# Kernel optimization log

Measured on AMD Instinct MI355X. Metric: run time of the kernel, lower is better.

## Reference

```python
import jax, jax.numpy as jnp
import numpy as np
import math

B, T, D = 4, 4096, 512

def setup_inputs() -> dict:
    key = jax.random.key(0)
    ks = jax.random.split(key, 6)
    scale = 1.0 / math.sqrt(D)
    return {
        "x": jax.random.normal(ks[0], (B, T, D), dtype=jnp.float32),
        "Wq": jax.random.normal(ks[1], (D, D), dtype=jnp.float32) * scale,
        "bq": jnp.zeros((D,), dtype=jnp.float32),
        "Wk": jax.random.normal(ks[2], (D, D), dtype=jnp.float32) * scale,
        "bk": jnp.zeros((D,), dtype=jnp.float32),
        "gamma": jax.random.normal(ks[3], (1,), dtype=jnp.float32) * 0.1,
    }

def reference(x, Wq, bq, Wk, bk, gamma):
    # Q = x @ Wq^T + bq ; K = x @ Wk^T + bk  (torch Linear convention: W [out,in])
    Q = jnp.einsum("btd,ed->bte", x, Wq) + bq  # [B,T,D]
    K = jnp.einsum("btd,ed->bte", x, Wk) + bk  # [B,T,D]
    scores = jnp.einsum("bqd,bkd->bqk", Q, K) / math.sqrt(D)  # [B,T,T]
    attn = jax.nn.softmax(scores, axis=-1)
    # dropout is identity in eval mode
    out = x + gamma * jnp.einsum("bqk,bkd->bqd", attn, x)
    return out
```

## Files before the change

kernel.cpp:

```cpp
#include <hip/hip_runtime.h>
#include <hip/hip_bf16.h>
#include <stdint.h>


#define B_ 4
#define T_ 4096
#define D_ 512

typedef short short8 __attribute__((ext_vector_type(8)));
typedef float f32x4 __attribute__((ext_vector_type(4)));

__device__ __forceinline__ unsigned short f2bf(float x) {
  union { float f; unsigned u; } v; v.f = x;
  unsigned r = v.u + 0x7fffu + ((v.u >> 16) & 1u);
  return (unsigned short)(r >> 16);
}
__device__ __forceinline__ unsigned char f2fp8(float x) {
  return (unsigned char)(__builtin_amdgcn_cvt_pk_fp8_f32(x, x, 0, false) & 0xff);
}
__device__ __forceinline__ float bf2f(unsigned short b) {
  union { unsigned u; float f; } v; v.u = ((unsigned)b) << 16; return v.f;
}

__device__ __forceinline__ void gload_lds16(const void* g, void* l) {
  __builtin_amdgcn_global_load_lds((const __attribute__((address_space(1))) void*)g,
                                   (__attribute__((address_space(3))) void*)l, 16, 0, 0);
}

__global__ __launch_bounds__(256) void cvt_w(const float* __restrict__ wq,
                                             const float* __restrict__ wk,
                                             unsigned short* __restrict__ oq,
                                             unsigned short* __restrict__ ok) {
  int i = (blockIdx.x * 256 + threadIdx.x) * 4;
  const float* s; unsigned short* d;
  if (i < 262144) { s = wq + i; d = oq + i; }
  else            { s = wk + (i - 262144); d = ok + (i - 262144); }
  float4 v = *(const float4*)s;
  ushort4 h; h.x = f2bf(v.x); h.y = f2bf(v.y); h.z = f2bf(v.z); h.w = f2bf(v.w);
  *(ushort4*)d = h;
}

__global__ __launch_bounds__(256) void prep_x(const float* __restrict__ x,
                                              unsigned short* __restrict__ xb,
                                              unsigned char* __restrict__ xV) {
  __shared__ unsigned short ldsT[64][72];
  int wg = blockIdx.x;
  int b = wg >> 9;
  int rem = wg & 511;
  int tt = rem >> 3, dt = rem & 7;
  int t0 = tt * 64, d0 = dt * 64;
  int tid = threadIdx.x;
  int p = tid & 15, rw = tid >> 4;
#pragma unroll
  for (int k = 0; k < 4; ++k) {
    int tr = rw + 16 * k;
    size_t off = ((size_t)(b * 4096 + t0 + tr)) * 512 + d0 + p * 4;
    float4 v = *(const float4*)(x + off);
    ushort4 h; h.x = f2bf(v.x); h.y = f2bf(v.y); h.z = f2bf(v.z); h.w = f2bf(v.w);
    *(ushort4*)(xb + off) = h;
    ldsT[p * 4 + 0][tr] = h.x; ldsT[p * 4 + 1][tr] = h.y;
    ldsT[p * 4 + 2][tr] = h.z; ldsT[p * 4 + 3][tr] = h.w;
  }
  __syncthreads();
#pragma unroll
  for (int k = 0; k < 4; ++k) {
    int dr = rw + 16 * k;
    float f0 = bf2f(ldsT[dr][p * 4 + 0]);
    float f1 = bf2f(ldsT[dr][p * 4 + 1]);
    float f2 = bf2f(ldsT[dr][p * 4 + 2]);
    float f3 = bf2f(ldsT[dr][p * 4 + 3]);
    unsigned pk = (unsigned)__builtin_amdgcn_cvt_pk_fp8_f32(f0, f1, 0, false);
    pk = (unsigned)__builtin_amdgcn_cvt_pk_fp8_f32(f2, f3, (int)pk, true);
    *(unsigned*)(xV + ((size_t)((b * 64 + tt) * 512 + d0 + dr)) * 64 + p * 4) = pk;
  }
}

__global__ __launch_bounds__(256, 2) void proj_gemm(const unsigned short* __restrict__ A,
                                                    const unsigned short* __restrict__ wq,
                                                    const unsigned short* __restrict__ wk,
                                                    const float* __restrict__ bq,
                                                    const float* __restrict__ bk,
                                                    unsigned char* __restrict__ Qo,
                                                    unsigned char* __restrict__ Ko) {
  __shared__ unsigned short As[2][8192];
  __shared__ unsigned short Bs[2][8192];
  const int tid = threadIdx.x;
  const int mt = blockIdx.x, nt = blockIdx.y, qk = blockIdx.z;
  const unsigned short* W = qk ? wk : wq;
  const float* bias = qk ? bk : bq;
  unsigned char* out = qk ? Ko : Qo;
  const int m0 = mt * 128, n0 = nt * 128;
  const int l = tid & 63, q15 = l & 15, g = l >> 4;
  const int w = tid >> 6, wm = w >> 1, wn = w & 1;

  auto stage = [&](int buf, int k0) {
#pragma unroll
    for (int j = 0; j < 4; ++j) {
      int chunk = j * 256 + tid;
      int row = chunk >> 3, cc = chunk & 7;
      int ccs = cc ^ (row & 7);
      gload_lds16(A + (size_t)(m0 + row) * 512 + k0 + ccs * 8, &As[buf][chunk * 8]);
      gload_lds16(W + (size_t)(n0 + row) * 512 + k0 + ccs * 8, &Bs[buf][chunk * 8]);
    }
  };
  stage(0, 0);
  __syncthreads();

  f32x4 acc[4][4] = {};
  for (int kt = 0; kt < 8; ++kt) {
    int cur = kt & 1;
    if (kt < 7) stage(cur ^ 1, (kt + 1) * 64);
#pragma unroll
    for (int ks = 0; ks < 2; ++ks) {
      short8 av[4], bv[4];
#pragma unroll
      for (int mf = 0; mf < 4; ++mf) {
        int row = 64 * wm + 16 * mf + q15;
        int cb = (ks * 64 + g * 16) ^ ((row & 7) << 4);
        av[mf] = *(const short8*)((const char*)&As[cur][0] + row * 128 + cb);
      }
#pragma unroll
      for (int nf = 0; nf < 4; ++nf) {
        int row = 64 * wn + 16 * nf + q15;
        int cb = (ks * 64 + g * 16) ^ ((row & 7) << 4);
        bv[nf] = *(const short8*)((const char*)&Bs[cur][0] + row * 128 + cb);
      }
#pragma unroll
      for (int mf = 0; mf < 4; ++mf)
#pragma unroll
        for (int nf = 0; nf < 4; ++nf)
          acc[mf][nf] = __builtin_amdgcn_mfma_f32_16x16x32_bf16(av[mf], bv[nf], acc[mf][nf], 0, 0, 0);
    }
    __syncthreads();
  }
#pragma unroll
  for (int nf = 0; nf < 4; ++nf) {
    int n = n0 + 64 * wn + 16 * nf + q15;
    float bv = bias[n];
#pragma unroll
    for (int mf = 0; mf < 4; ++mf) {
      int mbase = m0 + 64 * wm + 16 * mf + 4 * g;
#pragma unroll
      for (int r = 0; r < 4; ++r)
        out[(size_t)(mbase + r) * 512 + n] = f2fp8(acc[mf][nf][r] + bv);
    }
  }
}

__global__ __launch_bounds__(768, 3) void attn_kernel(const unsigned char* __restrict__ Qb,
                                                      const unsigned char* __restrict__ Kb,
                                                      const unsigned char* __restrict__ xV,
                                                      const float* __restrict__ x,
                                                      const float* __restrict__ gmp,
                                                      float* __restrict__ out) {
  extern __shared__ char smem[];
  unsigned char* Pl = (unsigned char*)(smem + 131072);
  float* scale_lds = (float*)(smem + 149504);
  float* lsum_lds  = (float*)(smem + 150016);
  unsigned* flags  = (unsigned*)(smem + 150272);

  const int hw = blockIdx.x;
  const int wg = (hw & 7) * 32 + (hw >> 3);
  const int b = wg >> 6, qt = wg & 63;
  const int tid = threadIdx.x;
  const int w = tid >> 6, l = tid & 63, q15 = l & 15, g = l >> 4;
  const float qscale = 0.04419417382415922f;

  const unsigned char* KbB = Kb + (size_t)b * 4096 * 512;
  const unsigned char* xVb = xV + (size_t)b * 64 * 512 * 64;

  auto stage = [&](int buf, int kt) {
    const unsigned char* src = KbB + (size_t)kt * 128 * 512;
    char* dst = smem + buf * 65536;
    int st = tid - 256;
#pragma unroll
    for (int j = 0; j < 8; ++j) {
      int ch = j * 512 + st;
      int r = ch >> 5, c = ch & 31;
      gload_lds16(src + (size_t)r * 512 + ((c ^ (r & 7)) << 4), dst + ch * 16);
    }
  };

  if (tid >= 256) stage(0, 0);
  __syncthreads();

  if (w < 4) {
    long qf_[16];
    {
      const unsigned char* Qrow =
          Qb + ((size_t)(b * 4096 + qt * 64 + 16 * w + q15)) * 512 + g * 8;
#pragma unroll
      for (int ds = 0; ds < 16; ++ds) qf_[ds] = *(const long*)(Qrow + ds * 32);
    }
    float mrun = -1e30f, lsum = 0.f;

#pragma unroll 1
    for (int s = 0; s <= 32; ++s) {
      if (s < 32) {
        const int cur = s & 1;
        f32x4 Sacc[8] = {};
        const char* kb = smem + cur * 65536;
        __builtin_amdgcn_s_setprio(1);
#pragma unroll
        for (int ds = 0; ds < 16; ++ds) {
          const int ch = 2 * ds + (g >> 1);
          const int half = (g & 1) << 3;
#pragma unroll
          for (int n = 0; n < 8; ++n) {
            int row = 16 * n + q15;
            long kf = *(const long*)(kb + row * 512 + ((ch ^ (row & 7)) << 4) + half);
            Sacc[n] = __builtin_amdgcn_mfma_f32_16x16x32_fp8_fp8(kf, qf_[ds], Sacc[n], 0, 0, 0);
          }
        }
        __builtin_amdgcn_s_setprio(0);
        float pmax = -1e30f;
#pragma unroll
        for (int n = 0; n < 8; ++n)
#pragma unroll
          for (int r = 0; r < 4; ++r) pmax = fmaxf(pmax, Sacc[n][r]);
        pmax = fmaxf(pmax, __shfl_xor(pmax, 16, 64));
        pmax = fmaxf(pmax, __shfl_xor(pmax, 32, 64));
        const float mnew = fmaxf(mrun, pmax);
        const float scl = __expf((mrun - mnew) * qscale);
        float psum = 0.f;
        unsigned char* Pp = Pl + cur * 9216 + (16 * w + q15) * 144 + 4 * g;
#pragma unroll
        for (int n = 0; n < 8; ++n) {
          float p0 = __expf((Sacc[n][0] - mnew) * qscale); psum += p0;
          float p1 = __expf((Sacc[n][1] - mnew) * qscale); psum += p1;
          float p2 = __expf((Sacc[n][2] - mnew) * qscale); psum += p2;
          float p3 = __expf((Sacc[n][3] - mnew) * qscale); psum += p3;
          unsigned pk = (unsigned)__builtin_amdgcn_cvt_pk_fp8_f32(p0, p1, 0, false);
          pk = (unsigned)__builtin_amdgcn_cvt_pk_fp8_f32(p2, p3, (int)pk, true);
          *(unsigned*)(Pp + 16 * n) = pk;
        }
        psum += __shfl_xor(psum, 16, 64);
        psum += __shfl_xor(psum, 32, 64);
        lsum = lsum * scl + psum;
        const bool nochg = (mnew == mrun);
        mrun = mnew;
        if (g == 0) scale_lds[cur * 64 + 16 * w + q15] = scl;
        if (s == 31 && g == 0) lsum_lds[16 * w + q15] = lsum;
        unsigned long long bal = __ballot(nochg ? 1 : 0);
        if (l == 0) flags[cur * 4 + w] = (bal == 0xFFFFFFFFFFFFFFFFull) ? 1u : 0u;
      }
      __syncthreads();
    }
  } else {
    const int pw = w - 4;
    f32x4 Oacc[4][4] = {};

#pragma unroll 1
    for (int s = 0; s <= 32; ++s) {
      if (s < 31) stage((s + 1) & 1, s + 1);
      if (s >= 1) {
        const int tv = s - 1;
        const int pcur = tv & 1;
        long vf[4][4];
#pragma unroll
        for (int f = 0; f < 4; ++f)
#pragma unroll
          for (int ks = 0; ks < 4; ++ks)
            vf[f][ks] = *(const long*)(xVb + (size_t)(2 * tv + (ks >> 1)) * 32768
                                       + (size_t)(64 * pw + 16 * f + q15) * 64
                                       + ((ks & 1) << 5) + g * 8);
        uint4 fv = *(const uint4*)&flags[pcur * 4];
        const bool skip = (fv.x & fv.y & fv.z & fv.w) != 0;
        const float* scp = scale_lds + pcur * 64;
        const unsigned char* Pb = Pl + pcur * 9216;
#pragma unroll
        for (int qf = 0; qf < 4; ++qf) {
          const unsigned char* prow = Pb + (16 * qf + q15) * 144 + g * 8;
          long pa[4];
#pragma unroll
          for (int ks = 0; ks < 4; ++ks) pa[ks] = *(const long*)(prow + 32 * ks);
          if (!skip) {
            float s0 = scp[16 * qf + 4 * g + 0];
            float s1 = scp[16 * qf + 4 * g + 1];
            float s2 = scp[16 * qf + 4 * g + 2];
            float s3 = scp[16 * qf + 4 * g + 3];
#pragma unroll
            for (int f = 0; f < 4; ++f) {
              Oacc[qf][f][0] *= s0; Oacc[qf][f][1] *= s1;
              Oacc[qf][f][2] *= s2; Oacc[qf][f][3] *= s3;
            }
          }
          __builtin_amdgcn_s_setprio(1);
#pragma unroll
          for (int f = 0; f < 4; ++f) {
            f32x4 a = Oacc[qf][f];
#pragma unroll
            for (int ks = 0; ks < 4; ++ks)
              a = __builtin_amdgcn_mfma_f32_16x16x32_fp8_fp8(pa[ks], vf[f][ks], a, 0, 0, 0);
            Oacc[qf][f] = a;
          }
          __builtin_amdgcn_s_setprio(0);
        }
      }
      __syncthreads();
    }

    const float gam = gmp[0];
#pragma unroll
    for (int qf = 0; qf < 4; ++qf) {
      float li0 = 1.f / lsum_lds[16 * qf + 4 * g + 0];
      float li1 = 1.f / lsum_lds[16 * qf + 4 * g + 1];
      float li2 = 1.f / lsum_lds[16 * qf + 4 * g + 2];
      float li3 = 1.f / lsum_lds[16 * qf + 4 * g + 3];
#pragma unroll
      for (int f = 0; f < 4; ++f) {
        int d = 64 * pw + 16 * f + q15;
        size_t base = ((size_t)(b * 4096 + qt * 64 + 16 * qf + 4 * g)) * 512 + d;
        f32x4 a = Oacc[qf][f];
        out[base]        = x[base]        + gam * a[0] * li0;
        out[base + 512]  = x[base + 512]  + gam * a[1] * li1;
        out[base + 1024] = x[base + 1024] + gam * a[2] * li2;
        out[base + 1536] = x[base + 1536] + gam * a[3] * li3;
      }
    }
  }
}

extern "C" void kernel_launch(void* const* d_in, const int* in_sizes, int n_in,
                              void* d_out, int out_size, void* d_ws, size_t ws_size,
                              hipStream_t stream) {
  (void)in_sizes; (void)n_in; (void)out_size; (void)ws_size;
  const float* x  = (const float*)d_in[0];
  const float* Wq = (const float*)d_in[1];
  const float* bq = (const float*)d_in[2];
  const float* Wk = (const float*)d_in[3];
  const float* bk = (const float*)d_in[4];
  const float* gm = (const float*)d_in[5];
  float* out = (float*)d_out;

  char* ws = (char*)d_ws;
  unsigned char*  Qb  = (unsigned char*)(ws);
  unsigned char*  Kb  = (unsigned char*)(ws + 8388608);
  unsigned char*  xV  = (unsigned char*)(ws + 16777216);
  unsigned short* xb  = (unsigned short*)(ws + 25165824);
  unsigned short* Wqb = (unsigned short*)(ws + 41943040);
  unsigned short* Wkb = (unsigned short*)(ws + 42467328);

  hipFuncSetAttribute((const void*)attn_kernel,
                      hipFuncAttributeMaxDynamicSharedMemorySize, 150304);

  cvt_w<<<512, 256, 0, stream>>>(Wq, Wk, Wqb, Wkb);
  prep_x<<<2048, 256, 0, stream>>>(x, xb, xV);
  proj_gemm<<<dim3(128, 4, 2), 256, 0, stream>>>(xb, Wqb, Wkb, bq, bk, Qb, Kb);
  attn_kernel<<<256, 768, 150304, stream>>>(Qb, Kb, xV, x, gm, out);
}
```

Baseline: 170.9 us.

## Use two QK waves with shared K fragments and register-staged K loads

Cuts the score-computing waves from four to two, each handling 32 query rows so every K fragment read from LDS feeds two MFMAs. K tiles are now loaded into registers by the PV waves and written to LDS with a new 8-byte XOR swizzle, replacing the direct global-to-LDS copies. The P buffer row padding shrinks and the block drops to 640 threads. The aim is less LDS read traffic for K and fewer waves. The risk is higher register pressure and serialised softmax work in the score waves, plus extra VGPR staging in the PV waves.

Result: slower. 276.3 us (+61.6%).

```diff
diff --git a/kernel.cpp b/kernel.cpp
--- a/kernel.cpp
+++ b/kernel.cpp
@@ -147,7 +147,7 @@
   }
 }
 
-__global__ __launch_bounds__(768, 3) void attn_kernel(const unsigned char* __restrict__ Qb,
+__global__ __launch_bounds__(640, 3) void attn_kernel(const unsigned char* __restrict__ Qb,
                                                       const unsigned char* __restrict__ Kb,
                                                       const unsigned char* __restrict__ xV,
                                                       const float* __restrict__ x,
@@ -155,9 +155,9 @@
                                                       float* __restrict__ out) {
   extern __shared__ char smem[];
   unsigned char* Pl = (unsigned char*)(smem + 131072);
-  float* scale_lds = (float*)(smem + 149504);
-  float* lsum_lds  = (float*)(smem + 150016);
-  unsigned* flags  = (unsigned*)(smem + 150272);
+  float* scale_lds = (float*)(smem + 148480);
+  float* lsum_lds  = (float*)(smem + 148992);
+  unsigned* flags  = (unsigned*)(smem + 149248);
 
   const int hw = blockIdx.x;
   const int wg = (hw & 7) * 32 + (hw >> 3);
@@ -169,94 +169,131 @@
   const unsigned char* KbB = Kb + (size_t)b * 4096 * 512;
   const unsigned char* xVb = xV + (size_t)b * 64 * 512 * 64;
 
-  auto stage = [&](int buf, int kt) {
-    const unsigned char* src = KbB + (size_t)kt * 128 * 512;
-    char* dst = smem + buf * 65536;
-    int st = tid - 256;
-#pragma unroll
-    for (int j = 0; j < 8; ++j) {
-      int ch = j * 512 + st;
-      int r = ch >> 5, c = ch & 31;
-      gload_lds16(src + (size_t)r * 512 + ((c ^ (r & 7)) << 4), dst + ch * 16);
-    }
-  };
-
-  if (tid >= 256) stage(0, 0);
+  if (tid >= 128) {
+    const int st = tid - 128, c = st & 63, w6 = st >> 6;
+    long kp[16];
+    const unsigned char* src = KbB + c * 8;
+#pragma unroll
+    for (int k = 0; k < 16; ++k)
+      kp[k] = *(const long*)(src + (size_t)(8 * k + w6) * 512);
+#pragma unroll
+    for (int k = 0; k < 16; ++k) {
+      int r = 8 * k + w6;
+      *(long*)(smem + r * 512 + ((c ^ (r & 15)) << 3)) = kp[k];
+    }
+  }
   __syncthreads();
 
-  if (w < 4) {
-    long qf_[16];
+  if (w < 2) {
+    long qf0[16], qf1[16];
     {
-      const unsigned char* Qrow =
-          Qb + ((size_t)(b * 4096 + qt * 64 + 16 * w + q15)) * 512 + g * 8;
-#pragma unroll
-      for (int ds = 0; ds < 16; ++ds) qf_[ds] = *(const long*)(Qrow + ds * 32);
-    }
-    float mrun = -1e30f, lsum = 0.f;
+      const unsigned char* Q0 =
+          Qb + ((size_t)(b * 4096 + qt * 64 + 32 * w + q15)) * 512 + g * 8;
+#pragma unroll
+      for (int ds = 0; ds < 16; ++ds) qf0[ds] = *(const long*)(Q0 + ds * 32);
+      const unsigned char* Q1 = Q0 + 16 * 512;
+#pragma unroll
+      for (int ds = 0; ds < 16; ++ds) qf1[ds] = *(const long*)(Q1 + ds * 32);
+    }
+    float mrun0 = -1e30f, mrun1 = -1e30f, lsum0 = 0.f, lsum1 = 0.f;
 
 #pragma unroll 1
     for (int s = 0; s <= 32; ++s) {
       if (s < 32) {
         const int cur = s & 1;
-        f32x4 Sacc[8] = {};
+        f32x4 S0[8] = {}, S1[8] = {};
         const char* kb = smem + cur * 65536;
         __builtin_amdgcn_s_setprio(1);
 #pragma unroll
         for (int ds = 0; ds < 16; ++ds) {
-          const int ch = 2 * ds + (g >> 1);
-          const int half = (g & 1) << 3;
 #pragma unroll
           for (int n = 0; n < 8; ++n) {
-            int row = 16 * n + q15;
-            long kf = *(const long*)(kb + row * 512 + ((ch ^ (row & 7)) << 4) + half);
-            Sacc[n] = __builtin_amdgcn_mfma_f32_16x16x32_fp8_fp8(kf, qf_[ds], Sacc[n], 0, 0, 0);
+            int r = 16 * n + q15;
+            long kf = *(const long*)(kb + r * 512 + ((((ds << 2) + g) ^ q15) << 3));
+            S0[n] = __builtin_amdgcn_mfma_f32_16x16x32_fp8_fp8(kf, qf0[ds], S0[n], 0, 0, 0);
+            S1[n] = __builtin_amdgcn_mfma_f32_16x16x32_fp8_fp8(kf, qf1[ds], S1[n], 0, 0, 0);
           }
         }
         __builtin_amdgcn_s_setprio(0);
-        float pmax = -1e30f;
-#pragma unroll
-        for (int n = 0; n < 8; ++n)
-#pragma unroll
-          for (int r = 0; r < 4; ++r) pmax = fmaxf(pmax, Sacc[n][r]);
-        pmax = fmaxf(pmax, __shfl_xor(pmax, 16, 64));
-        pmax = fmaxf(pmax, __shfl_xor(pmax, 32, 64));
-        const float mnew = fmaxf(mrun, pmax);
-        const float scl = __expf((mrun - mnew) * qscale);
-        float psum = 0.f;
-        unsigned char* Pp = Pl + cur * 9216 + (16 * w + q15) * 144 + 4 * g;
-#pragma unroll
-        for (int n = 0; n < 8; ++n) {
-          float p0 = __expf((Sacc[n][0] - mnew) * qscale); psum += p0;
-          float p1 = __expf((Sacc[n][1] - mnew) * qscale); psum += p1;
-          float p2 = __expf((Sacc[n][2] - mnew) * qscale); psum += p2;
-          float p3 = __expf((Sacc[n][3] - mnew) * qscale); psum += p3;
-          unsigned pk = (unsigned)__builtin_amdgcn_cvt_pk_fp8_f32(p0, p1, 0, false);
-          pk = (unsigned)__builtin_amdgcn_cvt_pk_fp8_f32(p2, p3, (int)pk, true);
-          *(unsigned*)(Pp + 16 * n) = pk;
+        bool nochg = true;
+        {
+          float pmax = -1e30f;
+#pragma unroll
+          for (int n = 0; n < 8; ++n)
+#pragma unroll
+            for (int r = 0; r < 4; ++r) pmax = fmaxf(pmax, S0[n][r]);
+          pmax = fmaxf(pmax, __shfl_xor(pmax, 16, 64));
+          pmax = fmaxf(pmax, __shfl_xor(pmax, 32, 64));
+          const float mnew = fmaxf(mrun0, pmax);
+          nochg = nochg && (mnew == mrun0);
+          const float scl = __expf((mrun0 - mnew) * qscale);
+          float psum = 0.f;
+          const int q_loc = 32 * w + q15;
+          unsigned char* Pp = Pl + cur * 8704 + q_loc * 136 + 4 * g;
+#pragma unroll
+          for (int n = 0; n < 8; ++n) {
+            float p0 = __expf((S0[n][0] - mnew) * qscale); psum += p0;
+            float p1 = __expf((S0[n][1] - mnew) * qscale); psum += p1;
+            float p2 = __expf((S0[n][2] - mnew) * qscale); psum += p2;
+            float p3 = __expf((S0[n][3] - mnew) * qscale); psum += p3;
+            unsigned pk = (unsigned)__builtin_amdgcn_cvt_pk_fp8_f32(p0, p1, 0, false);
+            pk = (unsigned)__builtin_amdgcn_cvt_pk_fp8_f32(p2, p3, (int)pk, true);
+            *(unsigned*)(Pp + 16 * n) = pk;
+          }
+          psum += __shfl_xor(psum, 16, 64);
+          psum += __shfl_xor(psum, 32, 64);
+          lsum0 = lsum0 * scl + psum;
+          mrun0 = mnew;
+          if (g == 0) scale_lds[cur * 64 + q_loc] = scl;
+          if (s == 31 && g == 0) lsum_lds[q_loc] = lsum0;
         }
-        psum += __shfl_xor(psum, 16, 64);
-        psum += __shfl_xor(psum, 32, 64);
-        lsum = lsum * scl + psum;
-        const bool nochg = (mnew == mrun);
-        mrun = mnew;
-        if (g == 0) scale_lds[cur * 64 + 16 * w + q15] = scl;
-        if (s == 31 && g == 0) lsum_lds[16 * w + q15] = lsum;
+        {
+          float pmax = -1e30f;
+#pragma unroll
+          for (int n = 0; n < 8; ++n)
+#pragma unroll
+            for (int r = 0; r < 4; ++r) pmax = fmaxf(pmax, S1[n][r]);
+          pmax = fmaxf(pmax, __shfl_xor(pmax, 16, 64));
+          pmax = fmaxf(pmax, __shfl_xor(pmax, 32, 64));
+          const float mnew = fmaxf(mrun1, pmax);
+          nochg = nochg && (mnew == mrun1);
+          const float scl = __expf((mrun1 - mnew) * qscale);
+          float psum = 0.f;
+          const int q_loc = 32 * w + 16 + q15;
+          unsigned char* Pp = Pl + cur * 8704 + q_loc * 136 + 4 * g;
+#pragma unroll
+          for (int n = 0; n < 8; ++n) {
+            float p0 = __expf((S1[n][0] - mnew) * qscale); psum += p0;
+            float p1 = __expf((S1[n][1] - mnew) * qscale); psum += p1;
+            float p2 = __expf((S1[n][2] - mnew) * qscale); psum += p2;
+            float p3 = __expf((S1[n][3] - mnew) * qscale); psum += p3;
+            unsigned pk = (unsigned)__builtin_amdgcn_cvt_pk_fp8_f32(p0, p1, 0, false);
+            pk = (unsigned)__builtin_amdgcn_cvt_pk_fp8_f32(p2, p3, (int)pk, true);
+            *(unsigned*)(Pp + 16 * n) = pk;
+          }
+          psum += __shfl_xor(psum, 16, 64);
+          psum += __shfl_xor(psum, 32, 64);
+          lsum1 = lsum1 * scl + psum;
+          mrun1 = mnew;
+          if (g == 0) scale_lds[cur * 64 + q_loc] = scl;
+          if (s == 31 && g == 0) lsum_lds[q_loc] = lsum1;
+        }
         unsigned long long bal = __ballot(nochg ? 1 : 0);
-        if (l == 0) flags[cur * 4 + w] = (bal == 0xFFFFFFFFFFFFFFFFull) ? 1u : 0u;
+        if (l == 0) flags[cur * 2 + w] = (bal == 0xFFFFFFFFFFFFFFFFull) ? 1u : 0u;
       }
       __syncthreads();
     }
   } else {
-    const int pw = w - 4;
+    const int pw = w - 2;
+    const int st = tid - 128, c = st & 63, w6 = st >> 6;
     f32x4 Oacc[4][4] = {};
 
 #pragma unroll 1
     for (int s = 0; s <= 32; ++s) {
-      if (s < 31) stage((s + 1) & 1, s + 1);
+      const int tv = s - 1;
+      const int pcur = tv & 1;
+      long vf[4][4];
       if (s >= 1) {
-        const int tv = s - 1;
-        const int pcur = tv & 1;
-        long vf[4][4];
 #pragma unroll
         for (int f = 0; f < 4; ++f)
 #pragma unroll
@@ -264,13 +301,22 @@
             vf[f][ks] = *(const long*)(xVb + (size_t)(2 * tv + (ks >> 1)) * 32768
                                        + (size_t)(64 * pw + 16 * f + q15) * 64
                                        + ((ks & 1) << 5) + g * 8);
-        uint4 fv = *(const uint4*)&flags[pcur * 4];
-        const bool skip = (fv.x & fv.y & fv.z & fv.w) != 0;
+      }
+      long kp[16];
+      if (s < 31) {
+        const unsigned char* src = KbB + (size_t)(s + 1) * 65536 + c * 8;
+#pragma unroll
+        for (int k = 0; k < 16; ++k)
+          kp[k] = *(const long*)(src + (size_t)(8 * k + w6) * 512);
+      }
+      if (s >= 1) {
+        uint2 fv = *(const uint2*)&flags[pcur * 2];
+        const bool skip = (fv.x & fv.y) != 0;
         const float* scp = scale_lds + pcur * 64;
-        const unsigned char* Pb = Pl + pcur * 9216;
+        const unsigned char* Pb = Pl + pcur * 8704;
 #pragma unroll
         for (int qf = 0; qf < 4; ++qf) {
-          const unsigned char* prow = Pb + (16 * qf + q15) * 144 + g * 8;
+          const unsigned char* prow = Pb + (16 * qf + q15) * 136 + g * 8;
           long pa[4];
 #pragma unroll
           for (int ks = 0; ks < 4; ++ks) pa[ks] = *(const long*)(prow + 32 * ks);
@@ -295,6 +341,14 @@
             Oacc[qf][f] = a;
           }
           __builtin_amdgcn_s_setprio(0);
+        }
+      }
+      if (s < 31) {
+        char* dst = smem + ((s + 1) & 1) * 65536;
+#pragma unroll
+        for (int k = 0; k < 16; ++k) {
+          int r = 8 * k + w6;
+          *(long*)(dst + r * 512 + ((c ^ (r & 15)) << 3)) = kp[k];
         }
       }
       __syncthreads();
@@ -342,10 +396,10 @@
   unsigned short* Wkb = (unsigned short*)(ws + 42467328);
 
   hipFuncSetAttribute((const void*)attn_kernel,
-                      hipFuncAttributeMaxDynamicSharedMemorySize, 150304);
+                      hipFuncAttributeMaxDynamicSharedMemorySize, 149264);
 
   cvt_w<<<512, 256, 0, stream>>>(Wq, Wk, Wqb, Wkb);
   prep_x<<<2048, 256, 0, stream>>>(x, xb, xV);
   proj_gemm<<<dim3(128, 4, 2), 256, 0, stream>>>(xb, Wqb, Wkb, bq, bk, Qb, Kb);
-  attn_kernel<<<256, 768, 150304, stream>>>(Qb, Kb, xV, x, gm, out);
-}
+  attn_kernel<<<256, 640, 149264, stream>>>(Qb, Kb, xV, x, gm, out);
+}
```
